# Kernel optimization log

Hardware: AMD Instinct MI355X
Metric: run time of the kernel (lower is better)

Reference implementation:

```python
import jax, jax.numpy as jnp
import numpy as np

BATCH = 64
NUM_BEAMS = 16
VOCAB = 128000
CUR_LEN = 8


def setup_inputs() -> dict:
    key = jax.random.key(0)
    k1, k2, k3 = jax.random.split(key, 3)
    rows = BATCH * NUM_BEAMS
    logits = jax.random.normal(k1, (rows, 1, VOCAB), dtype=jnp.float32)
    decoder_input_ids = jax.random.randint(k2, (rows, CUR_LEN), 0, VOCAB, dtype=jnp.int32)
    # mid-decode beam scores: arbitrary (negative-ish) cumulative log-probs
    beam_scores = jax.random.normal(k3, (rows,), dtype=jnp.float32)
    # arange(batch).repeat_interleave(num_beams) * num_beams
    beam_idx_offset = jnp.repeat(jnp.arange(BATCH, dtype=jnp.int32), NUM_BEAMS) * NUM_BEAMS
    return {
        "logits": logits,
        "decoder_input_ids": decoder_input_ids,
        "beam_scores": beam_scores,
        "beam_idx_offset": beam_idx_offset,
        "batch_size": BATCH,
        "num_beams": NUM_BEAMS,
    }


def reference(logits, decoder_input_ids, beam_scores, beam_idx_offset, batch_size, num_beams):
    # logits: [batch*beams, seq, vocab]; only the last position is used.
    vocab_size = logits.shape[-1]
    next_token_scores = jax.nn.log_softmax(logits[:, -1, :], axis=-1)  # [B*K, V]
    next_token_scores = next_token_scores + beam_scores[:, None]
    next_token_scores = next_token_scores.reshape(batch_size, num_beams * vocab_size)
    # top 2*K over the joint (beam, vocab) axis, sorted descending
    top_scores, top_idx = jax.lax.top_k(next_token_scores, 2 * num_beams)
    next_indices = top_idx // vocab_size  # source beam within batch
    next_tokens = top_idx % vocab_size    # token id
    new_beam_scores = top_scores[:, :num_beams].reshape(-1)           # [B*K]
    beam_next_tokens = next_tokens[:, :num_beams].reshape(-1)         # [B*K]
    beam_idx = next_indices[:, :num_beams].reshape(-1)                # [B*K]
    gathered = decoder_input_ids[beam_idx + beam_idx_offset, :]       # reorder beams
    new_decoder_input_ids = jnp.concatenate(
        [gathered, beam_next_tokens[:, None].astype(gathered.dtype)], axis=-1
    )
    return new_decoder_input_ids, new_beam_scores
```

## Files before the change

### kernel.cpp

```cpp
#include <hip/hip_runtime.h>
#include <cfloat>
#include <climits>

#define ROWS    1024
#define VOCABSZ 128000
#define NBEAMS  16
#define NBATCH  64
#define CURLEN  8
#define KTOP    16
#define WPB     4
#define SPLIT   2
#define BASE1   64512
#define TCAP    96
#define TGUARD  80
#define RCAP    (4 * TCAP)
#define RFLUSH  320
#define LOG2E   1.4426950408889634f
#define LN2     0.6931471805599453f
#define THRY    (3.10f * LOG2E)

#if __has_builtin(__builtin_amdgcn_exp2f)
#define EXP2(x) __builtin_amdgcn_exp2f(x)
#else
#define EXP2(x) exp2f(x)
#endif

__global__ __launch_bounds__(256, 8) void k1_scan(const float* __restrict__ logits,
                                                  float* __restrict__ wsS,
                                                  float* __restrict__ wsV,
                                                  int* __restrict__ wsI) {
    __shared__ float4 tup[WPB][TCAP];
    __shared__ int    tub[WPB][TCAP];
    __shared__ int    rbix[WPB][RCAP];
    __shared__ float  redS[WPB];
    __shared__ int    redC[WPB];

    const int gb    = blockIdx.x;
    const int row   = gb >> 1;
    const int blk   = gb & 1;
    const int ebase = blk ? BASE1 : 0;
    const int nstep = blk ? 62 : 63;
    const int t     = threadIdx.x;
    const int w     = t >> 6;
    const int lane  = t & 63;
    const float4* seg4 = reinterpret_cast<const float4*>(
        logits + (size_t)row * VOCABSZ + ebase);
    float* rbv = reinterpret_cast<float*>(&tup[w][0]);
    int*   rbi = &rbix[w][0];

    float s0 = 0.f, s1 = 0.f, s2 = 0.f, s3 = 0.f;
    float thr = THRY;
    int   cnt = 0;
    bool  ovf = false;

#define STEP(I, P) do {                                                        \
        const float y0 = (P).x * LOG2E, y1 = (P).y * LOG2E;                    \
        const float y2 = (P).z * LOG2E, y3 = (P).w * LOG2E;                    \
        s0 += EXP2(y0); s1 += EXP2(y1); s2 += EXP2(y2); s3 += EXP2(y3);        \
        const float mx = fmaxf(fmaxf(y0, y1), fmaxf(y2, y3));                  \
        if (__any(mx > thr)) {                                                 \
            const unsigned long long mk = __ballot(mx > thr);                  \
            const int pos = cnt + __popcll(mk & ((1ull << lane) - 1ull));      \
            if (mx > thr && pos < TCAP) {                                      \
                tup[w][pos] = make_float4(y0, y1, y2, y3);                     \
                tub[w][pos] = ebase + (I) * 1024 + t * 4;                      \
            }                                                                  \
            cnt += __popcll(mk);                                               \
            if (cnt > TGUARD) { ovf = true; thr = FLT_MAX; }                   \
        }                                                                      \
    } while (0)

    float4 A0 = seg4[0 * 256 + t];
    float4 A1 = seg4[1 * 256 + t];
    float4 A2 = seg4[2 * 256 + t];
    float4 A3 = seg4[3 * 256 + t];

    const int last = nstep - 1;
    #pragma unroll 1
    for (int g = 0; g < 15; ++g) {
        const int s4 = g * 4 + 4;
        const int i0 = (s4 + 0 < last) ? s4 + 0 : last;
        const int i1 = (s4 + 1 < last) ? s4 + 1 : last;
        const int i2 = (s4 + 2 < last) ? s4 + 2 : last;
        const int i3 = (s4 + 3 < last) ? s4 + 3 : last;
        const float4 N0 = seg4[i0 * 256 + t];
        const float4 N1 = seg4[i1 * 256 + t];
        const float4 N2 = seg4[i2 * 256 + t];
        const float4 N3 = seg4[i3 * 256 + t];

        STEP(g * 4 + 0, A0); STEP(g * 4 + 1, A1);
        STEP(g * 4 + 2, A2); STEP(g * 4 + 3, A3);

        A0 = N0; A1 = N1; A2 = N2; A3 = N3;
    }
    STEP(60, A0); STEP(61, A1);
    if (nstep == 63) STEP(62, A2);
#undef STEP


    float kv = -FLT_MAX; int ki = 0;
    auto do_flush = [&](int n) {
        kv = -FLT_MAX; ki = 0;
        for (int r = 0; r < KTOP; r++) {
            float bv = -FLT_MAX; int bi = INT_MAX; int bp = -1;
            for (int e = lane; e < n; e += 64) {
                const float v  = rbv[e];
                const int   ii = rbi[e];
                if (v > bv || (v == bv && ii < bi)) { bv = v; bi = ii; bp = e; }
            }
            for (int o = 32; o > 0; o >>= 1) {
                const float ov = __shfl_xor(bv, o);
                const int   oi = __shfl_xor(bi, o);
                const int   op = __shfl_xor(bp, o);
                if (ov > bv || (ov == bv && oi < bi)) { bv = ov; bi = oi; bp = op; }
            }
            if (lane == 0 && bp >= 0) rbv[bp] = -FLT_MAX;
            if (lane == r) { kv = bv; ki = bi; }
            thr = bv;
        }
    };

    const int nt = (cnt < TCAP) ? cnt : TCAP;
    int above = 0;
    for (int e = lane; e < nt; e += 64) {
        const float4 v = tup[w][e];
        const int    b = tub[w][e];
        above += (v.x > THRY) + (v.y > THRY) + (v.z > THRY) + (v.w > THRY);
        rbv[4 * e + 0] = v.x; rbi[4 * e + 0] = b + 0;
        rbv[4 * e + 1] = v.y; rbi[4 * e + 1] = b + 1;
        rbv[4 * e + 2] = v.z; rbi[4 * e + 2] = b + 2;
        rbv[4 * e + 3] = v.w; rbi[4 * e + 3] = b + 3;
    }
    for (int o = 32; o > 0; o >>= 1) above += __shfl_xor(above, o);

    float s = (s0 + s1) + (s2 + s3);
    for (int o = 32; o > 0; o >>= 1) s += __shfl_xor(s, o);
    if (lane == 0) { redS[w] = s; redC[w] = ovf ? -(1 << 20) : above; }
    __syncthreads();
    if (t == 0) wsS[gb] = (redS[0] + redS[1]) + (redS[2] + redS[3]);
    const int blockcnt = redC[0] + redC[1] + redC[2] + redC[3];

    int cnt4 = 4 * nt;
    if (blockcnt < KTOP) {
        thr = -FLT_MAX; cnt4 = 0;
        #pragma unroll 1
        for (int i = 0; i < nstep; ++i) {
            const float4 X = seg4[i * 256 + t];
            const float ys[4] = {X.x * LOG2E, X.y * LOG2E, X.z * LOG2E, X.w * LOG2E};
            #pragma unroll
            for (int j = 0; j < 4; ++j) {
                const bool pr = ys[j] > thr;
                const unsigned long long mk = __ballot(pr);
                if (mk) {
                    const int pos = cnt4 + __popcll(mk & ((1ull << lane) - 1ull));
                    if (pr && pos < RCAP) { rbv[pos] = ys[j]; rbi[pos] = ebase + i * 1024 + t * 4 + j; }
                    cnt4 += __popcll(mk);
                    if (cnt4 > RFLUSH) {
                        do_flush(cnt4);
                        if (lane < KTOP) { rbv[lane] = kv; rbi[lane] = ki; }
                        cnt4 = KTOP;
                    }
                }
            }
        }
    }

    do_flush(cnt4);

    if (lane < KTOP) {
        wsV[(size_t)row * 128 + blk * 64 + w * KTOP + lane] = kv;
        wsI[(size_t)row * 128 + blk * 64 + w * KTOP + lane] = ki;
    }
}

__global__ __launch_bounds__(64) void k2_select(const float* __restrict__ wsS,
                                                const float* __restrict__ wsV,
                                                const int* __restrict__ wsI,
                                                const float* __restrict__ beam_scores,
                                                const int* __restrict__ dec_ids,
                                                const int* __restrict__ beam_idx_offset,
                                                float* __restrict__ out) {
    const int batch = blockIdx.x;
    const int lane  = threadIdx.x;

    __shared__ float LSs[NBEAMS], BSs[NBEAMS];
    if (lane < NBEAMS) {
        const int row = batch * NBEAMS + lane;
        LSs[lane] = log2f(wsS[row * 2] + wsS[row * 2 + 1]);
        BSs[lane] = beam_scores[row];
    }
    __syncthreads();

    float sc[32]; int cb[32];
    #pragma unroll
    for (int p = 0; p < 32; p++) {
        const int slot = p * 64 + lane;
        const int rw   = slot >> 7;
        const int j    = slot & 127;
        const size_t base = (size_t)(batch * NBEAMS + rw) * 128 + j;
        const float v = wsV[base];
        const int idx = wsI[base];
        sc[p] = (v - LSs[rw]) * LN2 + BSs[rw];
        cb[p] = rw * VOCABSZ + idx;
    }

    unsigned int selmask = 0;
    float fs = 0.f; int fc = 0;
    for (int r = 0; r < KTOP; r++) {
        float bv = -FLT_MAX; int bi = INT_MAX; int bslot = -1;
        #pragma unroll
        for (int p = 0; p < 32; p++) {
            const bool avail = !((selmask >> p) & 1u);
            if (avail && (sc[p] > bv || (sc[p] == bv && cb[p] < bi))) {
                bv = sc[p]; bi = cb[p]; bslot = p;
            }
        }
        int bl = lane;
        for (int o = 32; o > 0; o >>= 1) {
            const float ov  = __shfl_xor(bv, o);
            const int   oi  = __shfl_xor(bi, o);
            const int   obl = __shfl_xor(bl, o);
            const int   obs = __shfl_xor(bslot, o);
            if (ov > bv || (ov == bv && oi < bi)) { bv = ov; bi = oi; bl = obl; bslot = obs; }
        }
        if (lane == bl) selmask |= (1u << bslot);
        if (lane == r) { fs = bv; fc = bi; }
    }

    if (lane < NBEAMS) {
        const int out_row = batch * NBEAMS + lane;
        const int beam  = fc / VOCABSZ;
        const int token = fc - beam * VOCABSZ;
        float* out0 = out;
        float* out1 = out + ROWS * (CURLEN + 1);
        out1[out_row] = fs;
        const int src = beam + beam_idx_offset[out_row];
        #pragma unroll
        for (int j = 0; j < CURLEN; j++)
            out0[out_row * (CURLEN + 1) + j] = (float)dec_ids[src * CURLEN + j];
        out0[out_row * (CURLEN + 1) + CURLEN] = (float)token;
    }
}

extern "C" void kernel_launch(void* const* d_in, const int* in_sizes, int n_in,
                              void* d_out, int out_size, void* d_ws, size_t ws_size,
                              hipStream_t stream) {
    const float* logits = (const float*)d_in[0];
    const int*   dec    = (const int*)d_in[1];
    const float* bscore = (const float*)d_in[2];
    const int*   bio    = (const int*)d_in[3];

    float* ws  = (float*)d_ws;
    float* wsS = ws;
    float* wsV = ws + ROWS * SPLIT;
    int*   wsI = (int*)(ws + ROWS * SPLIT + (size_t)ROWS * 128);

    k1_scan<<<ROWS * SPLIT, 256, 0, stream>>>(logits, wsS, wsV, wsI);
    k2_select<<<NBATCH, 64, 0, stream>>>(wsS, wsV, wsI, bscore, dec, bio,
                                         (float*)d_out);
}
```

Baseline: 150.7 us.

## Scan each row with one 512-thread block instead of two 256-thread blocks

The first kernel now assigns a whole vocabulary row to a single 8-wave block rather than splitting each row across two 4-wave blocks, with a tail step handled by the first 256 threads. The prefetch is restructured so each register is reloaded right after it is consumed, and the candidate threshold is raised so fewer elements go to the shared buffers. The per-row sum is written once and the select kernel reads it directly. Risks include fewer blocks in flight, dropped launch bounds affecting register allocation, and more rows falling into the slow rescan path if the higher threshold leaves fewer than 16 candidates.

```diff
diff --git a/kernel.cpp b/kernel.cpp
--- a/kernel.cpp
+++ b/kernel.cpp
@@ -8,16 +8,16 @@
 #define NBATCH  64
 #define CURLEN  8
 #define KTOP    16
-#define WPB     4
-#define SPLIT   2
-#define BASE1   64512
+#define WPB     8
+#define NFULL   62
+#define TAILB   31744
 #define TCAP    96
 #define TGUARD  80
 #define RCAP    (4 * TCAP)
 #define RFLUSH  320
 #define LOG2E   1.4426950408889634f
 #define LN2     0.6931471805599453f
-#define THRY    (3.10f * LOG2E)
+#define THRY    (3.30f * LOG2E)
 
 #if __has_builtin(__builtin_amdgcn_exp2f)
 #define EXP2(x) __builtin_amdgcn_exp2f(x)
@@ -25,26 +25,21 @@
 #define EXP2(x) exp2f(x)
 #endif
 
-__global__ __launch_bounds__(256, 8) void k1_scan(const float* __restrict__ logits,
-                                                  float* __restrict__ wsS,
-                                                  float* __restrict__ wsV,
-                                                  int* __restrict__ wsI) {
+__global__ void k1_scan(const float* __restrict__ logits,
+                        float* __restrict__ wsS,
+                        float* __restrict__ wsV,
+                        int* __restrict__ wsI) {
     __shared__ float4 tup[WPB][TCAP];
     __shared__ int    tub[WPB][TCAP];
     __shared__ int    rbix[WPB][RCAP];
     __shared__ float  redS[WPB];
     __shared__ int    redC[WPB];
 
-    const int gb    = blockIdx.x;
-    const int row   = gb >> 1;
-    const int blk   = gb & 1;
-    const int ebase = blk ? BASE1 : 0;
-    const int nstep = blk ? 62 : 63;
-    const int t     = threadIdx.x;
-    const int w     = t >> 6;
-    const int lane  = t & 63;
-    const float4* seg4 = reinterpret_cast<const float4*>(
-        logits + (size_t)row * VOCABSZ + ebase);
+    const int row  = blockIdx.x;
+    const int t    = threadIdx.x;
+    const int w    = t >> 6;
+    const int lane = t & 63;
+    const float4* seg4 = reinterpret_cast<const float4*>(logits + (size_t)row * VOCABSZ);
     float* rbv = reinterpret_cast<float*>(&tup[w][0]);
     int*   rbi = &rbix[w][0];
 
@@ -63,38 +58,31 @@
             const int pos = cnt + __popcll(mk & ((1ull << lane) - 1ull));      \
             if (mx > thr && pos < TCAP) {                                      \
                 tup[w][pos] = make_float4(y0, y1, y2, y3);                     \
-                tub[w][pos] = ebase + (I) * 1024 + t * 4;                      \
+                tub[w][pos] = (I) * 2048 + t * 4;                              \
             }                                                                  \
             cnt += __popcll(mk);                                               \
             if (cnt > TGUARD) { ovf = true; thr = FLT_MAX; }                   \
         }                                                                      \
     } while (0)
 
-    float4 A0 = seg4[0 * 256 + t];
-    float4 A1 = seg4[1 * 256 + t];
-    float4 A2 = seg4[2 * 256 + t];
-    float4 A3 = seg4[3 * 256 + t];
-
-    const int last = nstep - 1;
+    float4 A0 = seg4[0 * 512 + t];
+    float4 A1 = seg4[1 * 512 + t];
+    float4 A2 = seg4[2 * 512 + t];
+    float4 A3 = seg4[3 * 512 + t];
+
     #pragma unroll 1
     for (int g = 0; g < 15; ++g) {
-        const int s4 = g * 4 + 4;
-        const int i0 = (s4 + 0 < last) ? s4 + 0 : last;
-        const int i1 = (s4 + 1 < last) ? s4 + 1 : last;
-        const int i2 = (s4 + 2 < last) ? s4 + 2 : last;
-        const int i3 = (s4 + 3 < last) ? s4 + 3 : last;
-        const float4 N0 = seg4[i0 * 256 + t];
-        const float4 N1 = seg4[i1 * 256 + t];
-        const float4 N2 = seg4[i2 * 256 + t];
-        const float4 N3 = seg4[i3 * 256 + t];
-
-        STEP(g * 4 + 0, A0); STEP(g * 4 + 1, A1);
-        STEP(g * 4 + 2, A2); STEP(g * 4 + 3, A3);
-
-        A0 = N0; A1 = N1; A2 = N2; A3 = N3;
+        const int s = g * 4;
+        STEP(s + 0, A0); { const int n = (s + 4 < NFULL) ? s + 4 : NFULL - 1; A0 = seg4[n * 512 + t]; }
+        STEP(s + 1, A1); { const int n = (s + 5 < NFULL) ? s + 5 : NFULL - 1; A1 = seg4[n * 512 + t]; }
+        STEP(s + 2, A2); { const int n = (s + 6 < NFULL) ? s + 6 : NFULL - 1; A2 = seg4[n * 512 + t]; }
+        STEP(s + 3, A3); { const int n = (s + 7 < NFULL) ? s + 7 : NFULL - 1; A3 = seg4[n * 512 + t]; }
     }
     STEP(60, A0); STEP(61, A1);
-    if (nstep == 63) STEP(62, A2);
+    if (t < 256) {
+        const float4 X = seg4[TAILB + t];
+        STEP(62, X);
+    }
 #undef STEP
 
 
@@ -137,15 +125,23 @@
     for (int o = 32; o > 0; o >>= 1) s += __shfl_xor(s, o);
     if (lane == 0) { redS[w] = s; redC[w] = ovf ? -(1 << 20) : above; }
     __syncthreads();
-    if (t == 0) wsS[gb] = (redS[0] + redS[1]) + (redS[2] + redS[3]);
-    const int blockcnt = redC[0] + redC[1] + redC[2] + redC[3];
+    if (t == 0) {
+        float S = 0.f;
+        #pragma unroll
+        for (int i = 0; i < WPB; i++) S += redS[i];
+        wsS[row] = S;
+    }
+    int blockcnt = 0;
+    #pragma unroll
+    for (int i = 0; i < WPB; i++) blockcnt += redC[i];
 
     int cnt4 = 4 * nt;
     if (blockcnt < KTOP) {
         thr = -FLT_MAX; cnt4 = 0;
         #pragma unroll 1
-        for (int i = 0; i < nstep; ++i) {
-            const float4 X = seg4[i * 256 + t];
+        for (int i = 0; i <= NFULL; ++i) {
+            if (i == NFULL && t >= 256) break;
+            const float4 X = (i < NFULL) ? seg4[i * 512 + t] : seg4[TAILB + t];
             const float ys[4] = {X.x * LOG2E, X.y * LOG2E, X.z * LOG2E, X.w * LOG2E};
             #pragma unroll
             for (int j = 0; j < 4; ++j) {
@@ -153,7 +149,7 @@
                 const unsigned long long mk = __ballot(pr);
                 if (mk) {
                     const int pos = cnt4 + __popcll(mk & ((1ull << lane) - 1ull));
-                    if (pr && pos < RCAP) { rbv[pos] = ys[j]; rbi[pos] = ebase + i * 1024 + t * 4 + j; }
+                    if (pr && pos < RCAP) { rbv[pos] = ys[j]; rbi[pos] = i * 2048 + t * 4 + j; }
                     cnt4 += __popcll(mk);
                     if (cnt4 > RFLUSH) {
                         do_flush(cnt4);
@@ -168,8 +164,8 @@
     do_flush(cnt4);
 
     if (lane < KTOP) {
-        wsV[(size_t)row * 128 + blk * 64 + w * KTOP + lane] = kv;
-        wsI[(size_t)row * 128 + blk * 64 + w * KTOP + lane] = ki;
+        wsV[(size_t)row * 128 + w * KTOP + lane] = kv;
+        wsI[(size_t)row * 128 + w * KTOP + lane] = ki;
     }
 }
 
@@ -186,7 +182,7 @@
     __shared__ float LSs[NBEAMS], BSs[NBEAMS];
     if (lane < NBEAMS) {
         const int row = batch * NBEAMS + lane;
-        LSs[lane] = log2f(wsS[row * 2] + wsS[row * 2 + 1]);
+        LSs[lane] = log2f(wsS[row]);
         BSs[lane] = beam_scores[row];
     }
     __syncthreads();
@@ -252,10 +248,10 @@
 
     float* ws  = (float*)d_ws;
     float* wsS = ws;
-    float* wsV = ws + ROWS * SPLIT;
-    int*   wsI = (int*)(ws + ROWS * SPLIT + (size_t)ROWS * 128);
-
-    k1_scan<<<ROWS * SPLIT, 256, 0, stream>>>(logits, wsS, wsV, wsI);
+    float* wsV = ws + ROWS;
+    int*   wsI = (int*)(ws + ROWS + (size_t)ROWS * 128);
+
+    k1_scan<<<ROWS, 512, 0, stream>>>(logits, wsS, wsV, wsI);
     k2_select<<<NBATCH, 64, 0, stream>>>(wsS, wsV, wsI, bscore, dec, bio,
                                          (float*)d_out);
 }
```

Result: no change. 149.5 us (-0.8%).
